# Kernel tuning notes

Hardware: AMD Instinct MI355X
Metric: run time of the kernel (lower is better)

Reference implementation:

```python
import jax, jax.numpy as jnp
import numpy as np

B, T, F, H = 256, 128, 128, 512

def setup_inputs() -> dict:
    key = jax.random.key(0)
    ks = jax.random.split(key, 20)
    def xavier(k, shape):
        fan_in, fan_out = shape[1], shape[0]
        lim = np.sqrt(6.0 / (fan_in + fan_out)).astype(np.float32)
        return jax.random.uniform(k, shape, jnp.float32, -lim, lim)
    inp = {
        "x": jax.random.normal(ks[0], (B, T, F), jnp.float32),
        "m": (jax.random.uniform(ks[1], (B, T, F)) < 0.8).astype(jnp.float32),
        "d": jax.random.uniform(ks[2], (B, T, F), jnp.float32),
        "target_x": jax.random.normal(ks[3], (B, T, F), jnp.float32),
        "target_mask": (jax.random.uniform(ks[4], (B, T, F)) < 0.2).astype(jnp.float32),
        # TemporalDecay h: W [H,F], b [H]
        "td_h_W": xavier(ks[5], (H, F)), "td_h_b": jnp.zeros((H,), jnp.float32),
        # TemporalDecay x (diag): W [F,F], b [F]
        "td_x_W": xavier(ks[6], (F, F)), "td_x_b": jnp.zeros((F,), jnp.float32),
        # hist_reg Linear(H->F)
        "hist_W": xavier(ks[7], (F, H)), "hist_b": jnp.zeros((F,), jnp.float32),
        "feat_W": xavier(ks[8], (F, F)), "feat_b": jnp.zeros((F,), jnp.float32),
        # weight_combine Linear(2F->F)
        "wc_W": xavier(ks[9], (F, 2 * F)), "wc_b": jnp.zeros((F,), jnp.float32),
        # LSTMCell(2F -> H), PyTorch gate order i,f,g,o
        "W_ih": xavier(ks[10], (4 * H, 2 * F)), "W_hh": xavier(ks[11], (4 * H, H)),
        "b_ih": jnp.zeros((4 * H,), jnp.float32), "b_hh": jnp.zeros((4 * H,), jnp.float32),
    }
    return inp

def _rits_forward(x, m, d, target_x, target_mask,
                  td_h_W, td_h_b, td_x_W, td_x_b,
                  hist_W, hist_b, feat_W, feat_b, wc_W, wc_b,
                  W_ih, W_hh, b_ih, b_hh):
    Bx, Tx, Fx = x.shape
    Hx = td_h_W.shape[0]
    feat_mask = (1.0 - jnp.eye(Fx, dtype=x.dtype))
    feat_Wm_T = (feat_W * feat_mask).T              # [F,F]
    td_x_diag = jnp.diagonal(td_x_W)                # diag mask reduces matmul to elementwise

    def step(carry, inp):
        h, c, loss = carry
        x_t, m_t, d_t, tgt_t, ev_t = inp
        gamma_h = jnp.exp(-jax.nn.relu(d_t @ td_h_W.T + td_h_b))    # [B,H]
        gamma_x = jnp.exp(-jax.nn.relu(d_t * td_x_diag + td_x_b))   # [B,F]
        h = h * gamma_h
        x_hist = h @ hist_W.T + hist_b                              # [B,F]
        x_c = m_t * x_t + (1.0 - m_t) * x_hist
        z_h = x_c @ feat_Wm_T + feat_b
        alpha = jax.nn.sigmoid(jnp.concatenate([gamma_x, m_t], axis=1) @ wc_W.T + wc_b)
        c_h = alpha * z_h + (1.0 - alpha) * x_hist
        c_c = m_t * x_t + (1.0 - m_t) * c_h
        inputs = jnp.concatenate([c_c, m_t], axis=1)                # [B,2F]
        gates = inputs @ W_ih.T + b_ih + h @ W_hh.T + b_hh          # [B,4H]
        i_g, f_g, g_g, o_g = jnp.split(gates, 4, axis=1)
        c = jax.nn.sigmoid(f_g) * c + jax.nn.sigmoid(i_g) * jnp.tanh(g_g)
        h = jax.nn.sigmoid(o_g) * jnp.tanh(c)
        denom = ev_t.sum() + 1e-8
        loss = loss + (((x_hist - tgt_t) ** 2 * ev_t).sum()
                       + ((z_h - tgt_t) ** 2 * ev_t).sum()
                       + ((c_h - tgt_t) ** 2 * ev_t).sum()) / denom
        return (h, c, loss), c_c

    h0 = jnp.zeros((Bx, Hx), x.dtype)
    c0 = jnp.zeros((Bx, Hx), x.dtype)
    tm = lambda a: jnp.swapaxes(a, 0, 1)  # time-major [T,B,F]
    (_, _, loss), imps = jax.lax.scan(
        step, (h0, c0, jnp.float32(0.0)),
        (tm(x), tm(m), tm(d), tm(target_x), tm(target_mask)))
    imputations = jnp.swapaxes(imps, 0, 1)  # [B,T,F]
    return imputations, loss / max(Tx, 1)

def reference(x, m, d, target_x, target_mask,
              td_h_W, td_h_b, td_x_W, td_x_b,
              hist_W, hist_b, feat_W, feat_b, wc_W, wc_b,
              W_ih, W_hh, b_ih, b_hh):
    return _rits_forward(x, m, d, target_x, target_mask,
                         td_h_W, td_h_b, td_x_W, td_x_b,
                         hist_W, hist_b, feat_W, feat_b, wc_W, wc_b,
                         W_ih, W_hh, b_ih, b_hh)
```

## Files before the change

### kernel.cpp

```cpp
#include <hip/hip_runtime.h>

#define DEVINL __device__ __forceinline__

namespace {
constexpr int B = 256, T = 128, F = 128, H = 512;
constexpr int NBLK = 256;
constexpr int NTHR = 1024;

constexpr size_t OFF_NUM    = 0;
constexpr size_t OFF_DEN    = 128;
constexpr size_t OFF_WQCC   = 256;
constexpr size_t OFF_WQH    = OFF_WQCC + 64 * 2048;
constexpr size_t OFF_FSCC   = OFF_WQH + 128 * 2048;
constexpr size_t OFF_FSCHG  = OFF_FSCC + 2048;
constexpr size_t OFF_HISTQ  = OFF_FSCHG + 2048;
constexpr size_t OFF_FSCH   = OFF_HISTQ + 128 * 128;
constexpr size_t OFF_TD2    = OFF_FSCH + 128;
constexpr size_t OFF_FEAT2  = OFF_TD2 + 64 * 512;
constexpr size_t OFF_WC2    = OFF_FEAT2 + 64 * 128;
constexpr size_t OFF_BSUM   = OFF_WC2 + 128 * 128;
constexpr size_t OFF_FDIAG  = OFF_BSUM + 2048;
constexpr size_t WS_WORDS   = OFF_FDIAG + 128;

constexpr float ACT_S  = 15.875f;
constexpr float DEQ_CC = 1.f / (127.f * 15.875f);
constexpr float DEQ_H  = 1.f / (127.f * 127.f);
}

typedef _Float16 h2_t __attribute__((ext_vector_type(2)));

DEVINL h2_t as_h2(unsigned u) { union { unsigned u; h2_t h; } c; c.u = u; return c.h; }
DEVINL unsigned pack2(float a, float b) {
  union { h2_t h; unsigned u; } c;
  c.h = h2_t{(_Float16)a, (_Float16)b};
  return c.u;
}

#if defined(__has_builtin)
#if __has_builtin(__builtin_amdgcn_fdot2)
#define HAVE_FDOT2 1
#endif
#if __has_builtin(__builtin_amdgcn_sdot4)
#define HAVE_SDOT4 1
#endif
#endif
#ifdef HAVE_FDOT2
DEVINL float fdot2(h2_t a, h2_t b, float c) { return __builtin_amdgcn_fdot2(a, b, c, false); }
#else
DEVINL float fdot2(h2_t a, h2_t b, float c) {
  return fmaf((float)a.x, (float)b.x, fmaf((float)a.y, (float)b.y, c));
}
#endif
#ifdef HAVE_SDOT4
DEVINL int sdot4(int a, int b, int c) { return __builtin_amdgcn_sdot4(a, b, c, false); }
#else
DEVINL int sdot4(int a, int b, int c) {
  return c + ((a << 24) >> 24) * ((b << 24) >> 24)
           + ((a << 16) >> 24) * ((b << 16) >> 24)
           + ((a << 8) >> 24) * ((b << 8) >> 24)
           + (a >> 24) * (b >> 24);
}
#endif

DEVINL float fast_sig(float x)  { return 1.f / (1.f + __expf(-x)); }
DEVINL float fast_tanh(float x) { return 1.f - 2.f / (1.f + __expf(2.f * x)); }

DEVINL float wave_sum(float v) {
#pragma unroll
  for (int s = 32; s; s >>= 1) v += __shfl_down(v, s, 64);
  return v;
}
DEVINL float wave_max(float v) {
#pragma unroll
  for (int s = 32; s; s >>= 1) v = fmaxf(v, __shfl_down(v, s, 64));
  return v;
}

__global__ void prep_f16(const float* __restrict__ td_h_W, const float* __restrict__ feat_W,
                         const float* __restrict__ wc_W, const float* __restrict__ b_ih,
                         const float* __restrict__ b_hh,
                         unsigned* __restrict__ wsu, float* __restrict__ wsf) {
  int idx = blockIdx.x * blockDim.x + threadIdx.x;
  if (idx < 32768) {
    const int k2 = idx >> 9, j = idx & 511;
    wsu[OFF_TD2 + idx] = pack2(td_h_W[j * 128 + 2 * k2], td_h_W[j * 128 + 2 * k2 + 1]);
  } else if (idx < 40960) {
    const int i = idx - 32768, k2 = i >> 7, f = i & 127;
    wsu[OFF_FEAT2 + i] = pack2(feat_W[f * 128 + 2 * k2], feat_W[f * 128 + 2 * k2 + 1]);
  } else if (idx < 57344) {
    const int i = idx - 40960, k2 = i >> 7, f = i & 127;
    wsu[OFF_WC2 + i] = pack2(wc_W[f * 256 + 2 * k2], wc_W[f * 256 + 2 * k2 + 1]);
  } else if (idx < 59392) {
    const int i = idx - 57344, unit = i >> 2, g = i & 3;
    wsf[OFF_BSUM + i] = b_ih[g * 512 + unit] + b_hh[g * 512 + unit];
  } else if (idx < 59520) {
    const int f = idx - 59392;
    wsf[OFF_FDIAG + f] = (float)(_Float16)feat_W[f * 129];
  }
}

__global__ void prep_quant_wih(const float* __restrict__ Wih,
                               unsigned* __restrict__ wq, float* __restrict__ fscc) {
  const int col = blockIdx.x;
  const int unit = col >> 2, g = col & 3;
  const float* src = Wih + (size_t)(g * 512 + unit) * 256;
  const int t = threadIdx.x;
  const float4 v = ((const float4*)src)[t];
  float mx = fmaxf(fmaxf(fabsf(v.x), fabsf(v.y)), fmaxf(fabsf(v.z), fabsf(v.w)));
  mx = wave_max(mx);
  mx = __shfl(mx, 0, 64);
  const float s = (mx > 0.f) ? 127.f / mx : 0.f;
  const int q0 = __float2int_rn(v.x * s), q1 = __float2int_rn(v.y * s);
  const int q2 = __float2int_rn(v.z * s), q3 = __float2int_rn(v.w * s);
  wq[t * 2048 + col] =
      (q0 & 0xFF) | ((q1 & 0xFF) << 8) | ((q2 & 0xFF) << 16) | ((q3 & 0xFF) << 24);
  if (t == 0) fscc[col] = mx * DEQ_CC;
}

__global__ void prep_quant_whh(const float* __restrict__ Whh,
                               unsigned* __restrict__ wq, float* __restrict__ fschg) {
  const int col = blockIdx.x;
  const int unit = col >> 2, g = col & 3;
  const float* src = Whh + (size_t)(g * 512 + unit) * 512;
  const int t = threadIdx.x;
  const float4 v = ((const float4*)src)[t];
  float mx = fmaxf(fmaxf(fabsf(v.x), fabsf(v.y)), fmaxf(fabsf(v.z), fabsf(v.w)));
  mx = wave_max(mx);
  __shared__ float wm[2];
  if ((t & 63) == 0) wm[t >> 6] = mx;
  __syncthreads();
  const float maxv = fmaxf(wm[0], wm[1]);
  const float s = (maxv > 0.f) ? 127.f / maxv : 0.f;
  const int q0 = __float2int_rn(v.x * s), q1 = __float2int_rn(v.y * s);
  const int q2 = __float2int_rn(v.z * s), q3 = __float2int_rn(v.w * s);
  wq[t * 2048 + col] =
      (q0 & 0xFF) | ((q1 & 0xFF) << 8) | ((q2 & 0xFF) << 16) | ((q3 & 0xFF) << 24);
  if (t == 0) fschg[col] = maxv * DEQ_H;
}

__global__ void prep_quant_hist(const float* __restrict__ histW,
                                unsigned* __restrict__ histq, float* __restrict__ fsch) {
  const int f = blockIdx.x;
  const float* src = histW + (size_t)f * 512;
  const int t = threadIdx.x;
  const float4 v = ((const float4*)src)[t];
  float mx = fmaxf(fmaxf(fabsf(v.x), fabsf(v.y)), fmaxf(fabsf(v.z), fabsf(v.w)));
  mx = wave_max(mx);
  __shared__ float wm[2];
  if ((t & 63) == 0) wm[t >> 6] = mx;
  __syncthreads();
  const float maxv = fmaxf(wm[0], wm[1]);
  const float s = (maxv > 0.f) ? 127.f / maxv : 0.f;
  const int q0 = __float2int_rn(v.x * s), q1 = __float2int_rn(v.y * s);
  const int q2 = __float2int_rn(v.z * s), q3 = __float2int_rn(v.w * s);
  histq[t * 128 + f] =
      (q0 & 0xFF) | ((q1 & 0xFF) << 8) | ((q2 & 0xFF) << 16) | ((q3 & 0xFF) << 24);
  if (t == 0) fsch[f] = maxv * DEQ_H;
}

__global__ void __launch_bounds__(1024) rits_batch(
    const float* __restrict__ x, const float* __restrict__ m, const float* __restrict__ d,
    const float* __restrict__ tx, const float* __restrict__ tmask,
    const float* __restrict__ td_h_b, const float* __restrict__ td_x_W,
    const float* __restrict__ td_x_b, const float* __restrict__ hist_b,
    const float* __restrict__ feat_b, const float* __restrict__ wc_b,
    const unsigned* __restrict__ wsu, const float* __restrict__ wsf,
    float* __restrict__ num, float* __restrict__ den, float* __restrict__ out)
{
  const int tid = threadIdx.x;
  const int row = blockIdx.x;
  const int unit = tid & 511;
  const int kh = tid >> 9;

  __shared__ unsigned actq[64];
  __shared__ int hq[128];
  __shared__ unsigned d2[64];
  __shared__ unsigned xc2[64];
  __shared__ unsigned gxm2[128];
  __shared__ float xrow[128], mrow[128], drow[128], txrow[128], evrow[128];
  __shared__ int   partI[1024];
  __shared__ float partZ[1024], partA[1024];
  __shared__ int4  partHc[512], partHh[512];
  __shared__ float redA[2], redB[2];

  const float4 bs    = *(const float4*)(wsf + OFF_BSUM + 4 * unit);
  const float4 fscc4 = *(const float4*)(wsf + OFF_FSCC + 4 * unit);
  const float4 fsch4 = *(const float4*)(wsf + OFF_FSCHG + 4 * unit);
  const float tdb = td_h_b[unit];
  const int fc = tid & 127;
  const float hb = hist_b[fc], fb = feat_b[fc], wb = wc_b[fc];
  const float fd = wsf[OFF_FDIAG + fc];
  const float dxw = td_x_W[fc * 129], dxb = td_x_b[fc];
  const float fsch_f = wsf[OFF_FSCH + fc];

  float h0 = 0.f, c0 = 0.f;

  for (int t = 0; t < T; ++t) {
    const int base = (row * T + t) * F;
    float xh_r = 0.f, xc_r = 0.f;

    if (tid < 640) {
      const int a = tid >> 7, f = tid & 127;
      const float v = (a == 0 ? x[base + f] : a == 1 ? m[base + f] : a == 2 ? d[base + f]
                       : a == 3 ? tx[base + f] : tmask[base + f]);
      if      (a == 0) xrow[f]  = v;
      else if (a == 1) mrow[f]  = v;
      else if (a == 2) drow[f]  = v;
      else if (a == 3) txrow[f] = v;
      else             evrow[f] = v;
    } else if (tid < 704) {
      const int k2 = tid - 640;
      d2[k2] = pack2(d[base + 2 * k2], d[base + 2 * k2 + 1]);
    } else if (tid < 768) {
      const int q = tid - 704;
      gxm2[64 + q] = pack2(m[base + 2 * q], m[base + 2 * q + 1]);
    } else if (tid < 800) {
      const int w = tid - 768;
      const int b4 = base + 4 * w;
      const int q0 = __float2int_rn(m[b4] * ACT_S);
      const int q1 = __float2int_rn(m[b4 + 1] * ACT_S);
      const int q2 = __float2int_rn(m[b4 + 2] * ACT_S);
      const int q3 = __float2int_rn(m[b4 + 3] * ACT_S);
      actq[32 + w] =
          (q0 & 0xFF) | ((q1 & 0xFF) << 8) | ((q2 & 0xFF) << 16) | ((q3 & 0xFF) << 24);
    }
    __syncthreads();

    if (tid < 512) {
      float g0 = tdb;
#pragma unroll 8
      for (int k2 = 0; k2 < 64; ++k2)
        g0 = fdot2(as_h2(wsu[OFF_TD2 + (k2 << 9) + tid]), as_h2(d2[k2]), g0);
      h0 *= __expf(-fmaxf(g0, 0.f));
      int q = __float2int_rn(h0 * 127.f);
      const int a1 = __shfl_down(q, 1, 64), a2 = __shfl_down(q, 2, 64), a3 = __shfl_down(q, 3, 64);
      if ((tid & 3) == 0)
        hq[tid >> 2] =
            (q & 0xFF) | ((a1 & 0xFF) << 8) | ((a2 & 0xFF) << 16) | ((a3 & 0xFF) << 24);
    }
    __syncthreads();

    {
      const int kq = tid >> 7;
      int isum = 0;
#pragma unroll 8
      for (int k = 0; k < 16; ++k) {
        const int k4 = kq * 16 + k;
        isum = sdot4((int)wsu[OFF_HISTQ + (k4 << 7) + fc], hq[k4], isum);
      }
      partI[tid] = isum;
    }
    __syncthreads();

    if (tid < 128) {
      int isum = 0;
#pragma unroll
      for (int i = 0; i < 8; ++i) isum += partI[tid + 128 * i];
      xh_r = fmaf((float)isum, fsch_f, hb);
      const float gx = __expf(-fmaxf(fmaf(drow[tid], dxw, dxb), 0.f));
      const float mv = mrow[tid];
      xc_r = mv * xrow[tid] + (1.f - mv) * xh_r;
      const float xcs = __shfl_down(xc_r, 1, 64);
      const float gxs = __shfl_down(gx, 1, 64);
      if (!(tid & 1)) {
        xc2[tid >> 1]  = pack2(xc_r, xcs);
        gxm2[tid >> 1] = pack2(gx, gxs);
      }
    }
    __syncthreads();

    {
      const int kq = tid >> 7;
      float zs = 0.f;
#pragma unroll 8
      for (int k = 0; k < 8; ++k) {
        const int k2 = kq * 8 + k;
        zs = fdot2(as_h2(wsu[OFF_FEAT2 + (k2 << 7) + fc]), as_h2(xc2[k2]), zs);
      }
      partZ[tid] = zs;
      float as = 0.f;
#pragma unroll 8
      for (int k = 0; k < 16; ++k) {
        const int k2 = kq * 16 + k;
        as = fdot2(as_h2(wsu[OFF_WC2 + (k2 << 7) + fc]), as_h2(gxm2[k2]), as);
      }
      partA[tid] = as;
    }
    __syncthreads();

    if (tid < 128) {
      float z = fb, aa = wb;
#pragma unroll
      for (int i = 0; i < 8; ++i) { z += partZ[tid + 128 * i]; aa += partA[tid + 128 * i]; }
      z -= xc_r * fd;
      const float al = fast_sig(aa);
      const float ch = al * z + (1.f - al) * xh_r;
      const float mv = mrow[tid];
      const float cc = mv * xrow[tid] + (1.f - mv) * ch;
      out[base + tid] = cc;
      const float ev = evrow[tid], tg = txrow[tid];
      const float e1 = xh_r - tg, e2 = z - tg, e3 = ch - tg;
      const float s1 = wave_sum(ev * (e1 * e1 + e2 * e2 + e3 * e3));
      const float s2 = wave_sum(ev);
      if ((tid & 63) == 0) { redA[tid >> 6] = s1; redB[tid >> 6] = s2; }
      int qc = __float2int_rn(fminf(fmaxf(cc, -8.f), 8.f) * ACT_S);
      const int c1s = __shfl_down(qc, 1, 64), c2s = __shfl_down(qc, 2, 64), c3s = __shfl_down(qc, 3, 64);
      if (!(tid & 3))
        actq[tid >> 2] =
            (qc & 0xFF) | ((c1s & 0xFF) << 8) | ((c2s & 0xFF) << 16) | ((c3s & 0xFF) << 24);
    }
    __syncthreads();

    {
      if (tid == 1023) {
        atomicAdd(&num[t], redA[0] + redA[1]);
        atomicAdd(&den[t], redB[0] + redB[1]);
      }
      int ci = 0, cf = 0, cg = 0, co = 0;
      const unsigned* wq = wsu + OFF_WQCC + 4 * unit;
#pragma unroll 8
      for (int k = 0; k < 32; ++k) {
        const int k4 = kh * 32 + k;
        const uint4 w = *(const uint4*)(wq + (k4 << 11));
        const int a0 = (int)actq[k4];
        ci = sdot4((int)w.x, a0, ci); cf = sdot4((int)w.y, a0, cf);
        cg = sdot4((int)w.z, a0, cg); co = sdot4((int)w.w, a0, co);
      }
      int hi = 0, hf = 0, hg = 0, ho = 0;
      const unsigned* wh = wsu + OFF_WQH + 4 * unit;
#pragma unroll 8
      for (int k = 0; k < 64; ++k) {
        const int k4 = kh * 64 + k;
        const uint4 w = *(const uint4*)(wh + (k4 << 11));
        const int a0 = hq[k4];
        hi = sdot4((int)w.x, a0, hi); hf = sdot4((int)w.y, a0, hf);
        hg = sdot4((int)w.z, a0, hg); ho = sdot4((int)w.w, a0, ho);
      }
      if (tid >= 512) {
        partHc[unit] = int4{ci, cf, cg, co};
        partHh[unit] = int4{hi, hf, hg, ho};
      }
      __syncthreads();
      if (tid < 512) {
        const int4 pc = partHc[unit], ph = partHh[unit];
        const float ai = bs.x + fscc4.x * (float)(ci + pc.x) + fsch4.x * (float)(hi + ph.x);
        const float af = bs.y + fscc4.y * (float)(cf + pc.y) + fsch4.y * (float)(hf + ph.y);
        const float ag = bs.z + fscc4.z * (float)(cg + pc.z) + fsch4.z * (float)(hg + ph.z);
        const float ao = bs.w + fscc4.w * (float)(co + pc.w) + fsch4.w * (float)(ho + ph.w);
        const float ig = fast_sig(ai), fg = fast_sig(af);
        const float gg = fast_tanh(ag), og = fast_sig(ao);
        c0 = fg * c0 + ig * gg;
        h0 = og * fast_tanh(c0);
      }
    }
    __syncthreads();
  }
}

__global__ void finalize(const float* __restrict__ num, const float* __restrict__ den,
                         float* __restrict__ out) {
  __shared__ float red[2];
  const int t = threadIdx.x;
  float v = num[t] / (den[t] + 1e-8f);
  v = wave_sum(v);
  if ((t & 63) == 0) red[t >> 6] = v;
  __syncthreads();
  if (t == 0) out[(size_t)B * T * F] = (red[0] + red[1]) / (float)T;
}

extern "C" void kernel_launch(void* const* d_in, const int* in_sizes, int n_in,
                              void* d_out, int out_size, void* d_ws, size_t ws_size,
                              hipStream_t stream) {
  const float* x      = (const float*)d_in[0];
  const float* m      = (const float*)d_in[1];
  const float* d      = (const float*)d_in[2];
  const float* tx     = (const float*)d_in[3];
  const float* tmask  = (const float*)d_in[4];
  const float* td_h_W = (const float*)d_in[5];
  const float* td_h_b = (const float*)d_in[6];
  const float* td_x_W = (const float*)d_in[7];
  const float* td_x_b = (const float*)d_in[8];
  const float* hist_W = (const float*)d_in[9];
  const float* hist_b = (const float*)d_in[10];
  const float* feat_W = (const float*)d_in[11];
  const float* feat_b = (const float*)d_in[12];
  const float* wc_W   = (const float*)d_in[13];
  const float* wc_b   = (const float*)d_in[14];
  const float* W_ih   = (const float*)d_in[15];
  const float* W_hh   = (const float*)d_in[16];
  const float* b_ih   = (const float*)d_in[17];
  const float* b_hh   = (const float*)d_in[18];

  float*    wsf = (float*)d_ws;
  unsigned* wsu = (unsigned*)d_ws;
  float*    out = (float*)d_out;

  if (ws_size < WS_WORDS * 4) return;

  hipMemsetAsync(d_ws, 0, 256 * sizeof(float), stream);
  prep_f16<<<dim3((59520 + 255) / 256), dim3(256), 0, stream>>>(
      td_h_W, feat_W, wc_W, b_ih, b_hh, wsu, wsf);
  prep_quant_wih<<<dim3(2048), dim3(64), 0, stream>>>(
      W_ih, wsu + OFF_WQCC, wsf + OFF_FSCC);
  prep_quant_whh<<<dim3(2048), dim3(128), 0, stream>>>(
      W_hh, wsu + OFF_WQH, wsf + OFF_FSCHG);
  prep_quant_hist<<<dim3(128), dim3(128), 0, stream>>>(
      hist_W, wsu + OFF_HISTQ, wsf + OFF_FSCH);
  rits_batch<<<dim3(NBLK), dim3(NTHR), 0, stream>>>(
      x, m, d, tx, tmask, td_h_b, td_x_W, td_x_b, hist_b, feat_b, wc_b,
      wsu, wsf, wsf + OFF_NUM, wsf + OFF_DEN, out);
  finalize<<<dim3(1), dim3(128), 0, stream>>>(wsf + OFF_NUM, wsf + OFF_DEN, out);
}
```

Measured before the change: 2.436 ms.

## Split batch rows across cooperating block groups with MFMA int8 gates and global barriers

The main kernel now has groups of 16 blocks cooperate on 16 batch rows. Each block owns a slice of hidden units and features, keeps its LSTM weight fragments in registers, and computes gate matmuls with int8 MFMA instructions in place of per-thread sdot4 loops. Quantized h and imputed-c activations are exchanged through global memory, with atomic-counter barriers between groups at each timestep. The quantization prep kernels are fused and the weights re-laid out for MFMA fragments. The change aims to cut per-block weight streaming and raise matrix throughput. In exchange it adds several grid-level spin barriers per step and depends on all 256 blocks being co-resident.

Result: slower. 5.335 ms (+119.0%).

```diff
diff --git a/kernel.cpp b/kernel.cpp
--- a/kernel.cpp
+++ b/kernel.cpp
@@ -4,23 +4,25 @@
 
 namespace {
 constexpr int B = 256, T = 128, F = 128, H = 512;
-constexpr int NBLK = 256;
-constexpr int NTHR = 1024;
-
-constexpr size_t OFF_NUM    = 0;
-constexpr size_t OFF_DEN    = 128;
-constexpr size_t OFF_WQCC   = 256;
-constexpr size_t OFF_WQH    = OFF_WQCC + 64 * 2048;
-constexpr size_t OFF_FSCC   = OFF_WQH + 128 * 2048;
-constexpr size_t OFF_FSCHG  = OFF_FSCC + 2048;
-constexpr size_t OFF_HISTQ  = OFF_FSCHG + 2048;
-constexpr size_t OFF_FSCH   = OFF_HISTQ + 128 * 128;
-constexpr size_t OFF_TD2    = OFF_FSCH + 128;
-constexpr size_t OFF_FEAT2  = OFF_TD2 + 64 * 512;
-constexpr size_t OFF_WC2    = OFF_FEAT2 + 64 * 128;
-constexpr size_t OFF_BSUM   = OFF_WC2 + 128 * 128;
-constexpr size_t OFF_FDIAG  = OFF_BSUM + 2048;
-constexpr size_t WS_WORDS   = OFF_FDIAG + 128;
+constexpr int NBLK = 256, NTHR = 1024;
+
+constexpr size_t OFF_NUM   = 0;
+constexpr size_t OFF_DEN   = 128;
+constexpr size_t OFF_CTR   = 256;
+constexpr size_t OFF_WQF   = 320;
+constexpr size_t OFF_FSCC  = OFF_WQF + 393216;
+constexpr size_t OFF_FSCHG = OFF_FSCC + 2048;
+constexpr size_t OFF_HISTQ = OFF_FSCHG + 2048;
+constexpr size_t OFF_FSCH  = OFF_HISTQ + 16384;
+constexpr size_t OFF_TD2   = OFF_FSCH + 128;
+constexpr size_t OFF_FEAT2 = OFF_TD2 + 32768;
+constexpr size_t OFF_WC2   = OFF_FEAT2 + 8192;
+constexpr size_t OFF_BSUM  = OFF_WC2 + 16384;
+constexpr size_t OFF_FDIAG = OFF_BSUM + 2048;
+constexpr size_t OFF_HQB   = OFF_FDIAG + 128;
+constexpr size_t OFF_XCB   = OFF_HQB + 65536;
+constexpr size_t OFF_CCB   = OFF_XCB + 32768;
+constexpr size_t WS_WORDS  = OFF_CCB + 16384;
 
 constexpr float ACT_S  = 15.875f;
 constexpr float DEQ_CC = 1.f / (127.f * 15.875f);
@@ -28,6 +30,7 @@
 }
 
 typedef _Float16 h2_t __attribute__((ext_vector_type(2)));
+typedef int v4i __attribute__((ext_vector_type(4)));
 
 DEVINL h2_t as_h2(unsigned u) { union { unsigned u; h2_t h; } c; c.u = u; return c.h; }
 DEVINL unsigned pack2(float a, float b) {
@@ -76,19 +79,44 @@
   return v;
 }
 
+DEVINL unsigned agload(const unsigned* p) {
+  return __hip_atomic_load(p, __ATOMIC_RELAXED, __HIP_MEMORY_SCOPE_AGENT);
+}
+DEVINL unsigned long long agload64(const unsigned long long* p) {
+  return __hip_atomic_load(p, __ATOMIC_RELAXED, __HIP_MEMORY_SCOPE_AGENT);
+}
+DEVINL void agstore(unsigned* p, unsigned v) {
+  __hip_atomic_store(p, v, __ATOMIC_RELAXED, __HIP_MEMORY_SCOPE_AGENT);
+}
+
+DEVINL void group_barrier(unsigned* ctr, unsigned target) {
+  __syncthreads();
+  if (threadIdx.x == 0) {
+    __threadfence();
+    __hip_atomic_fetch_add(ctr, 1u, __ATOMIC_RELEASE, __HIP_MEMORY_SCOPE_AGENT);
+    unsigned v = __hip_atomic_load(ctr, __ATOMIC_ACQUIRE, __HIP_MEMORY_SCOPE_AGENT);
+    int guard = 0;
+    while (v < target && ++guard < (1 << 24)) {
+      __builtin_amdgcn_s_sleep(1);
+      v = __hip_atomic_load(ctr, __ATOMIC_ACQUIRE, __HIP_MEMORY_SCOPE_AGENT);
+    }
+  }
+  __syncthreads();
+}
+
 __global__ void prep_f16(const float* __restrict__ td_h_W, const float* __restrict__ feat_W,
                          const float* __restrict__ wc_W, const float* __restrict__ b_ih,
                          const float* __restrict__ b_hh,
                          unsigned* __restrict__ wsu, float* __restrict__ wsf) {
-  int idx = blockIdx.x * blockDim.x + threadIdx.x;
+  const int idx = blockIdx.x * blockDim.x + threadIdx.x;
   if (idx < 32768) {
-    const int k2 = idx >> 9, j = idx & 511;
-    wsu[OFF_TD2 + idx] = pack2(td_h_W[j * 128 + 2 * k2], td_h_W[j * 128 + 2 * k2 + 1]);
+    const int u = idx >> 6, k2 = idx & 63;
+    wsu[OFF_TD2 + idx] = pack2(td_h_W[u * 128 + 2 * k2], td_h_W[u * 128 + 2 * k2 + 1]);
   } else if (idx < 40960) {
-    const int i = idx - 32768, k2 = i >> 7, f = i & 127;
+    const int i = idx - 32768, f = i >> 6, k2 = i & 63;
     wsu[OFF_FEAT2 + i] = pack2(feat_W[f * 128 + 2 * k2], feat_W[f * 128 + 2 * k2 + 1]);
   } else if (idx < 57344) {
-    const int i = idx - 40960, k2 = i >> 7, f = i & 127;
+    const int i = idx - 40960, f = i >> 7, k2 = i & 127;
     wsu[OFF_WC2 + i] = pack2(wc_W[f * 256 + 2 * k2], wc_W[f * 256 + 2 * k2 + 1]);
   } else if (idx < 59392) {
     const int i = idx - 57344, unit = i >> 2, g = i & 3;
@@ -99,47 +127,48 @@
   }
 }
 
-__global__ void prep_quant_wih(const float* __restrict__ Wih,
-                               unsigned* __restrict__ wq, float* __restrict__ fscc) {
-  const int col = blockIdx.x;
-  const int unit = col >> 2, g = col & 3;
-  const float* src = Wih + (size_t)(g * 512 + unit) * 256;
-  const int t = threadIdx.x;
-  const float4 v = ((const float4*)src)[t];
-  float mx = fmaxf(fmaxf(fabsf(v.x), fabsf(v.y)), fmaxf(fabsf(v.z), fabsf(v.w)));
-  mx = wave_max(mx);
-  mx = __shfl(mx, 0, 64);
-  const float s = (mx > 0.f) ? 127.f / mx : 0.f;
+DEVINL unsigned q4pack(float4 v, float s) {
   const int q0 = __float2int_rn(v.x * s), q1 = __float2int_rn(v.y * s);
   const int q2 = __float2int_rn(v.z * s), q3 = __float2int_rn(v.w * s);
-  wq[t * 2048 + col] =
-      (q0 & 0xFF) | ((q1 & 0xFF) << 8) | ((q2 & 0xFF) << 16) | ((q3 & 0xFF) << 24);
-  if (t == 0) fscc[col] = mx * DEQ_CC;
-}
-
-__global__ void prep_quant_whh(const float* __restrict__ Whh,
-                               unsigned* __restrict__ wq, float* __restrict__ fschg) {
+  return (q0 & 0xFF) | ((q1 & 0xFF) << 8) | ((q2 & 0xFF) << 16) | ((q3 & 0xFF) << 24);
+}
+
+__global__ void prep_gates(const float* __restrict__ Wih, const float* __restrict__ Whh,
+                           unsigned* __restrict__ wsu, float* __restrict__ wsf) {
   const int col = blockIdx.x;
-  const int unit = col >> 2, g = col & 3;
-  const float* src = Whh + (size_t)(g * 512 + unit) * 512;
-  const int t = threadIdx.x;
-  const float4 v = ((const float4*)src)[t];
-  float mx = fmaxf(fmaxf(fabsf(v.x), fabsf(v.y)), fmaxf(fabsf(v.z), fabsf(v.w)));
-  mx = wave_max(mx);
-  __shared__ float wm[2];
-  if ((t & 63) == 0) wm[t >> 6] = mx;
-  __syncthreads();
-  const float maxv = fmaxf(wm[0], wm[1]);
-  const float s = (maxv > 0.f) ? 127.f / maxv : 0.f;
-  const int q0 = __float2int_rn(v.x * s), q1 = __float2int_rn(v.y * s);
-  const int q2 = __float2int_rn(v.z * s), q3 = __float2int_rn(v.w * s);
-  wq[t * 2048 + col] =
-      (q0 & 0xFF) | ((q1 & 0xFF) << 8) | ((q2 & 0xFF) << 16) | ((q3 & 0xFF) << 24);
-  if (t == 0) fschg[col] = maxv * DEQ_H;
-}
-
-__global__ void prep_quant_hist(const float* __restrict__ histW,
-                                unsigned* __restrict__ histq, float* __restrict__ fsch) {
+  const int unit = col >> 2, g = col & 3, t = threadIdx.x;
+  const float* si = Wih + (size_t)(g * 512 + unit) * 256;
+  const float* sh = Whh + (size_t)(g * 512 + unit) * 512;
+  const float4 vi = ((const float4*)si)[t];
+  const float4 va = ((const float4*)sh)[t];
+  const float4 vb = ((const float4*)sh)[t + 64];
+  float mi = fmaxf(fmaxf(fabsf(vi.x), fabsf(vi.y)), fmaxf(fabsf(vi.z), fabsf(vi.w)));
+  float mh = fmaxf(fmaxf(fmaxf(fabsf(va.x), fabsf(va.y)), fmaxf(fabsf(va.z), fabsf(va.w))),
+                   fmaxf(fmaxf(fabsf(vb.x), fabsf(vb.y)), fmaxf(fabsf(vb.z), fabsf(vb.w))));
+  mi = wave_max(mi); mh = wave_max(mh);
+  mi = __shfl(mi, 0, 64); mh = __shfl(mh, 0, 64);
+  const float ssi = (mi > 0.f) ? 127.f / mi : 0.f;
+  const float ssh = (mh > 0.f) ? 127.f / mh : 0.f;
+  if (t == 0) { wsf[OFF_FSCC + col] = mi * DEQ_CC; wsf[OFF_FSCHG + col] = mh * DEQ_H; }
+
+  const int mid = col >> 7, nl = (col >> 4) & 7, c15 = col & 15;
+  const int q = (t >> 2) & 3, r = t & 3;
+  {
+    const int kt = t >> 4, kh = kt >> 1, loc = (kt & 1) * 4 + r;
+    const size_t a = ((size_t)((((mid * 8 + nl) * 2 + kh) * 64) + q * 16 + c15)) * 24 + loc;
+    wsu[OFF_WQF + a] = q4pack(vi, ssi);
+  }
+#pragma unroll
+  for (int p = 0; p < 2; ++p) {
+    const int k4 = t + 64 * p;
+    const int kt = k4 >> 4, kh = kt >> 2, loc = 8 + (kt & 3) * 4 + r;
+    const size_t a = ((size_t)((((mid * 8 + nl) * 2 + kh) * 64) + q * 16 + c15)) * 24 + loc;
+    wsu[OFF_WQF + a] = q4pack(p ? vb : va, ssh);
+  }
+}
+
+__global__ void prep_hist(const float* __restrict__ histW,
+                          unsigned* __restrict__ wsu, float* __restrict__ wsf) {
   const int f = blockIdx.x;
   const float* src = histW + (size_t)f * 512;
   const int t = threadIdx.x;
@@ -151,207 +180,276 @@
   __syncthreads();
   const float maxv = fmaxf(wm[0], wm[1]);
   const float s = (maxv > 0.f) ? 127.f / maxv : 0.f;
-  const int q0 = __float2int_rn(v.x * s), q1 = __float2int_rn(v.y * s);
-  const int q2 = __float2int_rn(v.z * s), q3 = __float2int_rn(v.w * s);
-  histq[t * 128 + f] =
-      (q0 & 0xFF) | ((q1 & 0xFF) << 8) | ((q2 & 0xFF) << 16) | ((q3 & 0xFF) << 24);
-  if (t == 0) fsch[f] = maxv * DEQ_H;
-}
-
-__global__ void __launch_bounds__(1024) rits_batch(
+  wsu[OFF_HISTQ + (size_t)f * 128 + t] = q4pack(v, s);
+  if (t == 0) wsf[OFF_FSCH + f] = maxv * DEQ_H;
+}
+
+__global__ void __launch_bounds__(NTHR) rits_group(
     const float* __restrict__ x, const float* __restrict__ m, const float* __restrict__ d,
     const float* __restrict__ tx, const float* __restrict__ tmask,
     const float* __restrict__ td_h_b, const float* __restrict__ td_x_W,
     const float* __restrict__ td_x_b, const float* __restrict__ hist_b,
     const float* __restrict__ feat_b, const float* __restrict__ wc_b,
-    const unsigned* __restrict__ wsu, const float* __restrict__ wsf,
+    unsigned* __restrict__ ws, const float* __restrict__ wsf,
     float* __restrict__ num, float* __restrict__ den, float* __restrict__ out)
 {
   const int tid = threadIdx.x;
-  const int row = blockIdx.x;
-  const int unit = tid & 511;
-  const int kh = tid >> 9;
-
-  __shared__ unsigned actq[64];
-  __shared__ int hq[128];
-  __shared__ unsigned d2[64];
-  __shared__ unsigned xc2[64];
-  __shared__ unsigned gxm2[128];
-  __shared__ float xrow[128], mrow[128], drow[128], txrow[128], evrow[128];
-  __shared__ int   partI[1024];
-  __shared__ float partZ[1024], partA[1024];
-  __shared__ int4  partHc[512], partHh[512];
-  __shared__ float redA[2], redB[2];
-
-  const float4 bs    = *(const float4*)(wsf + OFF_BSUM + 4 * unit);
-  const float4 fscc4 = *(const float4*)(wsf + OFF_FSCC + 4 * unit);
-  const float4 fsch4 = *(const float4*)(wsf + OFF_FSCHG + 4 * unit);
-  const float tdb = td_h_b[unit];
-  const int fc = tid & 127;
-  const float hb = hist_b[fc], fb = feat_b[fc], wb = wc_b[fc];
-  const float fd = wsf[OFF_FDIAG + fc];
-  const float dxw = td_x_W[fc * 129], dxb = td_x_b[fc];
-  const float fsch_f = wsf[OFF_FSCH + fc];
-
-  float h0 = 0.f, c0 = 0.f;
+  const int grp = blockIdx.x & 15, mid = blockIdx.x >> 4;
+  const int r0g = grp << 4, u0 = mid << 5, f0 = mid << 3, c0 = mid << 7;
+  const int lane = tid & 63, wv = tid >> 6;
+  const int nl = wv >> 1, kh = wv & 1;
+  const int m15 = lane & 15, lg = lane >> 4, swA = (m15 & 3) << 2;
+
+  __shared__ __align__(16) unsigned tdl_s[32 * 68];
+  __shared__ __align__(16) unsigned histl_s[8 * 132];
+  __shared__ __align__(16) unsigned featl_s[8 * 68];
+  __shared__ __align__(16) unsigned wcl_s[8 * 132];
+  __shared__ __align__(16) unsigned hq_s[16 * 132];
+  __shared__ __align__(16) unsigned actq_s[16 * 68];
+  __shared__ float h_s[16 * 33], c_s[16 * 33];
+  __shared__ float dxw_s[128], dxb_s[128];
+  __shared__ __align__(16) unsigned arena32[4800];
+
+  unsigned* d2_a   = arena32;
+  unsigned* xc2_a  = arena32 + 1088;
+  unsigned* gxm2_a = arena32 + 2176;
+  float* xsl  = (float*)(arena32 + 4288);
+  float* txsl = (float*)(arena32 + 4416);
+  float* evsl = (float*)(arena32 + 4544);
+  float* msl  = (float*)(arena32 + 4672);
+  float* gb   = (float*)arena32;
+
+  const unsigned* wqf = ws + OFF_WQF +
+      (size_t)((((mid << 3) + nl) * 2 + kh) * 64 + lane) * 24;
+  const v4i bcc0 = *(const v4i*)(wqf + 0),  bcc1 = *(const v4i*)(wqf + 4);
+  const v4i bh0  = *(const v4i*)(wqf + 8),  bh1  = *(const v4i*)(wqf + 12);
+  const v4i bh2  = *(const v4i*)(wqf + 16), bh3  = *(const v4i*)(wqf + 20);
+
+  const int colg = c0 + (nl << 4) + m15;
+  const float fscc_r = wsf[OFF_FSCC + colg];
+  const float fsch_r = wsf[OFF_FSCHG + colg];
+  const float bs_r   = wsf[OFF_BSUM + colg];
+
+  float tdb = 0.f;
+  if (tid < 512) tdb = td_h_b[u0 + (tid >> 4)];
+  float hb = 0.f, fb = 0.f, wb = 0.f, fd = 0.f, fsf = 0.f;
+  if (tid < 128) {
+    const int f = f0 + (tid & 7);
+    hb = hist_b[f]; fb = feat_b[f]; wb = wc_b[f];
+    fd = wsf[OFF_FDIAG + f]; fsf = wsf[OFF_FSCH + f];
+  }
+
+  {
+    if (tid < 512) {
+      const int u = tid >> 4, w4 = (tid & 15) << 2;
+#pragma unroll
+      for (int i = 0; i < 4; ++i)
+        tdl_s[u * 68 + w4 + i] = ws[OFF_TD2 + (size_t)(u0 + u) * 64 + w4 + i];
+      featl_s[(tid >> 6) * 68 + (tid & 63)] =
+          ws[OFF_FEAT2 + (size_t)(f0 + (tid >> 6)) * 64 + (tid & 63)];
+    }
+    histl_s[(tid >> 7) * 132 + (tid & 127)] =
+        ws[OFF_HISTQ + (size_t)(f0 + (tid >> 7)) * 128 + (tid & 127)];
+    wcl_s[(tid >> 7) * 132 + (tid & 127)] =
+        ws[OFF_WC2 + (size_t)(f0 + (tid >> 7)) * 128 + (tid & 127)];
+    if (tid < 128) { dxw_s[tid] = td_x_W[tid * 129]; dxb_s[tid] = td_x_b[tid]; }
+    if (tid < 528) { h_s[tid] = 0.f; c_s[tid] = 0.f; }
+  }
+  __syncthreads();
+
+  unsigned* ctr = ws + OFF_CTR + grp * 3;
 
   for (int t = 0; t < T; ++t) {
-    const int base = (row * T + t) * F;
-    float xh_r = 0.f, xc_r = 0.f;
-
-    if (tid < 640) {
-      const int a = tid >> 7, f = tid & 127;
-      const float v = (a == 0 ? x[base + f] : a == 1 ? m[base + f] : a == 2 ? d[base + f]
-                       : a == 3 ? tx[base + f] : tmask[base + f]);
-      if      (a == 0) xrow[f]  = v;
-      else if (a == 1) mrow[f]  = v;
-      else if (a == 2) drow[f]  = v;
-      else if (a == 3) txrow[f] = v;
-      else             evrow[f] = v;
-    } else if (tid < 704) {
-      const int k2 = tid - 640;
-      d2[k2] = pack2(d[base + 2 * k2], d[base + 2 * k2 + 1]);
-    } else if (tid < 768) {
-      const int q = tid - 704;
-      gxm2[64 + q] = pack2(m[base + 2 * q], m[base + 2 * q + 1]);
-    } else if (tid < 800) {
-      const int w = tid - 768;
-      const int b4 = base + 4 * w;
-      const int q0 = __float2int_rn(m[b4] * ACT_S);
-      const int q1 = __float2int_rn(m[b4 + 1] * ACT_S);
-      const int q2 = __float2int_rn(m[b4 + 2] * ACT_S);
-      const int q3 = __float2int_rn(m[b4 + 3] * ACT_S);
-      actq[32 + w] =
-          (q0 & 0xFF) | ((q1 & 0xFF) << 8) | ((q2 & 0xFF) << 16) | ((q3 & 0xFF) << 24);
+    const int par = t & 1;
+    unsigned* hqb = ws + OFF_HQB + (size_t)((par * 16 + grp) * 16) * 128;
+    unsigned* xcb = ws + OFF_XCB + (size_t)((par * 16 + grp) * 16) * 64;
+    unsigned* ccb = ws + OFF_CCB + (size_t)((par * 16 + grp) * 16) * 32;
+    const unsigned tgt = 16u * (unsigned)(t + 1);
+
+    float xh = 0.f, xc = 0.f, mvv = 0.f, xvv = 0.f;
+
+    {
+      const int r = tid >> 6, j = tid & 63;
+      const size_t base = ((size_t)(r0g + r) * T + t) * F;
+      const float dv0 = d[base + 2 * j], dv1 = d[base + 2 * j + 1];
+      d2_a[r * 68 + j] = pack2(dv0, dv1);
+      const float gx0 = __expf(-fmaxf(fmaf(dv0, dxw_s[2 * j], dxb_s[2 * j]), 0.f));
+      const float gx1 = __expf(-fmaxf(fmaf(dv1, dxw_s[2 * j + 1], dxb_s[2 * j + 1]), 0.f));
+      gxm2_a[r * 132 + j] = pack2(gx0, gx1);
+      const float mv0 = m[base + 2 * j], mv1 = m[base + 2 * j + 1];
+      gxm2_a[r * 132 + 64 + j] = pack2(mv0, mv1);
+      if (j < 32) {
+        const int q0 = __float2int_rn(m[base + 4 * j] * ACT_S);
+        const int q1 = __float2int_rn(m[base + 4 * j + 1] * ACT_S);
+        const int q2 = __float2int_rn(m[base + 4 * j + 2] * ACT_S);
+        const int q3 = __float2int_rn(m[base + 4 * j + 3] * ACT_S);
+        actq_s[r * 68 + ((32 + j) ^ ((r & 3) << 2))] =
+            (q0 & 0xFF) | ((q1 & 0xFF) << 8) | ((q2 & 0xFF) << 16) | ((q3 & 0xFF) << 24);
+        const int k = j & 7, sel = j >> 3;
+        const float v = (sel == 0) ? x[base + f0 + k] : (sel == 1) ? tx[base + f0 + k]
+                      : (sel == 2) ? tmask[base + f0 + k] : m[base + f0 + k];
+        if (sel == 0) xsl[r * 8 + k] = v;
+        else if (sel == 1) txsl[r * 8 + k] = v;
+        else if (sel == 2) evsl[r * 8 + k] = v;
+        else msl[r * 8 + k] = v;
+      }
     }
     __syncthreads();
 
     if (tid < 512) {
+      const int u = tid >> 4, r = tid & 15;
       float g0 = tdb;
+      const uint4* tw = (const uint4*)(tdl_s + u * 68);
+      const uint4* dw = (const uint4*)(d2_a + r * 68);
+#pragma unroll
+      for (int q = 0; q < 16; ++q) {
+        const uint4 w = tw[q], dd = dw[q];
+        g0 = fdot2(as_h2(w.x), as_h2(dd.x), g0);
+        g0 = fdot2(as_h2(w.y), as_h2(dd.y), g0);
+        g0 = fdot2(as_h2(w.z), as_h2(dd.z), g0);
+        g0 = fdot2(as_h2(w.w), as_h2(dd.w), g0);
+      }
+      const float hv = h_s[r * 33 + u] * __expf(-fmaxf(g0, 0.f));
+      h_s[r * 33 + u] = hv;
+      int q = __float2int_rn(hv * 127.f);
+      const int a1 = __shfl_down(q, 16, 64), a2 = __shfl_down(q, 32, 64),
+                a3 = __shfl_down(q, 48, 64);
+      if (!(u & 3))
+        agstore(hqb + r * 128 + (u0 >> 2) + (u >> 2),
+                (q & 0xFF) | ((a1 & 0xFF) << 8) | ((a2 & 0xFF) << 16) | ((a3 & 0xFF) << 24));
+    }
+    group_barrier(ctr + 0, tgt);
+
+    {
+      const int r = tid >> 6, w0 = (tid & 63) << 1;
+      const unsigned long long v =
+          agload64((const unsigned long long*)(hqb + r * 128 + w0));
+      const int swr = (r & 3) << 2;
+      hq_s[r * 132 + (w0 ^ swr)] = (unsigned)v;
+      hq_s[r * 132 + ((w0 | 1) ^ swr)] = (unsigned)(v >> 32);
+    }
+    __syncthreads();
+
+    if (tid < 128) {
+      const int r = tid >> 3, fl = tid & 7;
+      int isum = 0;
+      const uint4* hw = (const uint4*)(histl_s + fl * 132);
+      const int swr = (r & 3) << 2;
 #pragma unroll 8
-      for (int k2 = 0; k2 < 64; ++k2)
-        g0 = fdot2(as_h2(wsu[OFF_TD2 + (k2 << 9) + tid]), as_h2(d2[k2]), g0);
-      h0 *= __expf(-fmaxf(g0, 0.f));
-      int q = __float2int_rn(h0 * 127.f);
-      const int a1 = __shfl_down(q, 1, 64), a2 = __shfl_down(q, 2, 64), a3 = __shfl_down(q, 3, 64);
-      if ((tid & 3) == 0)
-        hq[tid >> 2] =
-            (q & 0xFF) | ((a1 & 0xFF) << 8) | ((a2 & 0xFF) << 16) | ((a3 & 0xFF) << 24);
+      for (int qq = 0; qq < 32; ++qq) {
+        const uint4 w = hw[qq];
+        const int4 hv = *(const int4*)(hq_s + r * 132 + (((qq) << 2) ^ swr));
+        isum = sdot4((int)w.x, hv.x, isum);
+        isum = sdot4((int)w.y, hv.y, isum);
+        isum = sdot4((int)w.z, hv.z, isum);
+        isum = sdot4((int)w.w, hv.w, isum);
+      }
+      xh = fmaf((float)isum, fsf, hb);
+      mvv = msl[r * 8 + fl]; xvv = xsl[r * 8 + fl];
+      xc = mvv * xvv + (1.f - mvv) * xh;
+      const float xcs = __shfl_down(xc, 1, 64);
+      if (!(fl & 1)) agstore(xcb + r * 64 + ((f0 + fl) >> 1), pack2(xc, xcs));
+    }
+    group_barrier(ctr + 1, tgt);
+
+    {
+      const int r = tid >> 6, w = tid & 63;
+      xc2_a[r * 68 + w] = agload(xcb + r * 64 + w);
     }
     __syncthreads();
 
+    if (tid < 128) {
+      const int r = tid >> 3, fl = tid & 7;
+      float z = fb, aa = wb;
+      {
+        const uint4* fw = (const uint4*)(featl_s + fl * 68);
+        const uint4* xw = (const uint4*)(xc2_a + r * 68);
+#pragma unroll 8
+        for (int qq = 0; qq < 16; ++qq) {
+          const uint4 w = fw[qq], x4 = xw[qq];
+          z = fdot2(as_h2(w.x), as_h2(x4.x), z);
+          z = fdot2(as_h2(w.y), as_h2(x4.y), z);
+          z = fdot2(as_h2(w.z), as_h2(x4.z), z);
+          z = fdot2(as_h2(w.w), as_h2(x4.w), z);
+        }
+        const uint4* ww = (const uint4*)(wcl_s + fl * 132);
+        const uint4* gw = (const uint4*)(gxm2_a + r * 132);
+#pragma unroll 8
+        for (int qq = 0; qq < 32; ++qq) {
+          const uint4 w = ww[qq], g4 = gw[qq];
+          aa = fdot2(as_h2(w.x), as_h2(g4.x), aa);
+          aa = fdot2(as_h2(w.y), as_h2(g4.y), aa);
+          aa = fdot2(as_h2(w.z), as_h2(g4.z), aa);
+          aa = fdot2(as_h2(w.w), as_h2(g4.w), aa);
+        }
+      }
+      z -= xc * fd;
+      const float al = fast_sig(aa);
+      const float ch = al * z + (1.f - al) * xh;
+      const float cc = mvv * xvv + (1.f - mvv) * ch;
+      out[((size_t)(r0g + r) * T + t) * F + f0 + fl] = cc;
+      const float tg = txsl[r * 8 + fl], evv = evsl[r * 8 + fl];
+      const float e1 = xh - tg, e2 = z - tg, e3 = ch - tg;
+      const float s1 = wave_sum(evv * (e1 * e1 + e2 * e2 + e3 * e3));
+      const float s2 = wave_sum(evv);
+      if (!(tid & 63)) { atomicAdd(&num[t], s1); atomicAdd(&den[t], s2); }
+      int qc = __float2int_rn(fminf(fmaxf(cc, -8.f), 8.f) * ACT_S);
+      const int c1 = __shfl_down(qc, 1, 64), c2 = __shfl_down(qc, 2, 64),
+                c3 = __shfl_down(qc, 3, 64);
+      if (!(fl & 3))
+        agstore(ccb + r * 32 + ((f0 + fl) >> 2),
+                (qc & 0xFF) | ((c1 & 0xFF) << 8) | ((c2 & 0xFF) << 16) | ((c3 & 0xFF) << 24));
+    }
+
+    v4i accH = {0, 0, 0, 0};
     {
-      const int kq = tid >> 7;
-      int isum = 0;
-#pragma unroll 8
-      for (int k = 0; k < 16; ++k) {
-        const int k4 = kq * 16 + k;
-        isum = sdot4((int)wsu[OFF_HISTQ + (k4 << 7) + fc], hq[k4], isum);
+      const unsigned* hrow = hq_s + m15 * 132;
+      const v4i a0 = *(const v4i*)(hrow + ((((kh * 4 + 0) << 4) + (lg << 2)) ^ swA));
+      accH = __builtin_amdgcn_mfma_i32_16x16x64_i8(a0, bh0, accH, 0, 0, 0);
+      const v4i a1 = *(const v4i*)(hrow + ((((kh * 4 + 1) << 4) + (lg << 2)) ^ swA));
+      accH = __builtin_amdgcn_mfma_i32_16x16x64_i8(a1, bh1, accH, 0, 0, 0);
+      const v4i a2 = *(const v4i*)(hrow + ((((kh * 4 + 2) << 4) + (lg << 2)) ^ swA));
+      accH = __builtin_amdgcn_mfma_i32_16x16x64_i8(a2, bh2, accH, 0, 0, 0);
+      const v4i a3 = *(const v4i*)(hrow + ((((kh * 4 + 3) << 4) + (lg << 2)) ^ swA));
+      accH = __builtin_amdgcn_mfma_i32_16x16x64_i8(a3, bh3, accH, 0, 0, 0);
+    }
+    group_barrier(ctr + 2, tgt);
+
+    if (tid < 512) {
+      const int r = tid >> 5, w = tid & 31;
+      actq_s[r * 68 + (w ^ ((r & 3) << 2))] = agload(ccb + r * 32 + w);
+    }
+    __syncthreads();
+
+    {
+      v4i accC = {0, 0, 0, 0};
+      const unsigned* arow = actq_s + m15 * 68;
+      const v4i a0 = *(const v4i*)(arow + ((((kh * 2 + 0) << 4) + (lg << 2)) ^ swA));
+      accC = __builtin_amdgcn_mfma_i32_16x16x64_i8(a0, bcc0, accC, 0, 0, 0);
+      const v4i a1 = *(const v4i*)(arow + ((((kh * 2 + 1) << 4) + (lg << 2)) ^ swA));
+      accC = __builtin_amdgcn_mfma_i32_16x16x64_i8(a1, bcc1, accC, 0, 0, 0);
+      float* gbp = gb + (size_t)((kh << 7) + (nl << 4) + m15) * 18 + (lg << 2);
+      const float badd = kh ? 0.f : bs_r;
+      gbp[0] = fmaf(fscc_r, (float)accC[0], fmaf(fsch_r, (float)accH[0], badd));
+      gbp[1] = fmaf(fscc_r, (float)accC[1], fmaf(fsch_r, (float)accH[1], badd));
+      gbp[2] = fmaf(fscc_r, (float)accC[2], fmaf(fsch_r, (float)accH[2], badd));
+      gbp[3] = fmaf(fscc_r, (float)accC[3], fmaf(fsch_r, (float)accH[3], badd));
+    }
+    __syncthreads();
+
+    if (tid < 512) {
+      const int ul = tid >> 4, r = tid & 15;
+      float a4[4];
+#pragma unroll
+      for (int gg = 0; gg < 4; ++gg) {
+        const int cl = ul * 4 + gg;
+        a4[gg] = gb[(size_t)cl * 18 + r] + gb[(size_t)(128 + cl) * 18 + r];
       }
-      partI[tid] = isum;
-    }
-    __syncthreads();
-
-    if (tid < 128) {
-      int isum = 0;
-#pragma unroll
-      for (int i = 0; i < 8; ++i) isum += partI[tid + 128 * i];
-      xh_r = fmaf((float)isum, fsch_f, hb);
-      const float gx = __expf(-fmaxf(fmaf(drow[tid], dxw, dxb), 0.f));
-      const float mv = mrow[tid];
-      xc_r = mv * xrow[tid] + (1.f - mv) * xh_r;
-      const float xcs = __shfl_down(xc_r, 1, 64);
-      const float gxs = __shfl_down(gx, 1, 64);
-      if (!(tid & 1)) {
-        xc2[tid >> 1]  = pack2(xc_r, xcs);
-        gxm2[tid >> 1] = pack2(gx, gxs);
-      }
-    }
-    __syncthreads();
-
-    {
-      const int kq = tid >> 7;
-      float zs = 0.f;
-#pragma unroll 8
-      for (int k = 0; k < 8; ++k) {
-        const int k2 = kq * 8 + k;
-        zs = fdot2(as_h2(wsu[OFF_FEAT2 + (k2 << 7) + fc]), as_h2(xc2[k2]), zs);
-      }
-      partZ[tid] = zs;
-      float as = 0.f;
-#pragma unroll 8
-      for (int k = 0; k < 16; ++k) {
-        const int k2 = kq * 16 + k;
-        as = fdot2(as_h2(wsu[OFF_WC2 + (k2 << 7) + fc]), as_h2(gxm2[k2]), as);
-      }
-      partA[tid] = as;
-    }
-    __syncthreads();
-
-    if (tid < 128) {
-      float z = fb, aa = wb;
-#pragma unroll
-      for (int i = 0; i < 8; ++i) { z += partZ[tid + 128 * i]; aa += partA[tid + 128 * i]; }
-      z -= xc_r * fd;
-      const float al = fast_sig(aa);
-      const float ch = al * z + (1.f - al) * xh_r;
-      const float mv = mrow[tid];
-      const float cc = mv * xrow[tid] + (1.f - mv) * ch;
-      out[base + tid] = cc;
-      const float ev = evrow[tid], tg = txrow[tid];
-      const float e1 = xh_r - tg, e2 = z - tg, e3 = ch - tg;
-      const float s1 = wave_sum(ev * (e1 * e1 + e2 * e2 + e3 * e3));
-      const float s2 = wave_sum(ev);
-      if ((tid & 63) == 0) { redA[tid >> 6] = s1; redB[tid >> 6] = s2; }
-      int qc = __float2int_rn(fminf(fmaxf(cc, -8.f), 8.f) * ACT_S);
-      const int c1s = __shfl_down(qc, 1, 64), c2s = __shfl_down(qc, 2, 64), c3s = __shfl_down(qc, 3, 64);
-      if (!(tid & 3))
-        actq[tid >> 2] =
-            (qc & 0xFF) | ((c1s & 0xFF) << 8) | ((c2s & 0xFF) << 16) | ((c3s & 0xFF) << 24);
-    }
-    __syncthreads();
-
-    {
-      if (tid == 1023) {
-        atomicAdd(&num[t], redA[0] + redA[1]);
-        atomicAdd(&den[t], redB[0] + redB[1]);
-      }
-      int ci = 0, cf = 0, cg = 0, co = 0;
-      const unsigned* wq = wsu + OFF_WQCC + 4 * unit;
-#pragma unroll 8
-      for (int k = 0; k < 32; ++k) {
-        const int k4 = kh * 32 + k;
-        const uint4 w = *(const uint4*)(wq + (k4 << 11));
-        const int a0 = (int)actq[k4];
-        ci = sdot4((int)w.x, a0, ci); cf = sdot4((int)w.y, a0, cf);
-        cg = sdot4((int)w.z, a0, cg); co = sdot4((int)w.w, a0, co);
-      }
-      int hi = 0, hf = 0, hg = 0, ho = 0;
-      const unsigned* wh = wsu + OFF_WQH + 4 * unit;
-#pragma unroll 8
-      for (int k = 0; k < 64; ++k) {
-        const int k4 = kh * 64 + k;
-        const uint4 w = *(const uint4*)(wh + (k4 << 11));
-        const int a0 = hq[k4];
-        hi = sdot4((int)w.x, a0, hi); hf = sdot4((int)w.y, a0, hf);
-        hg = sdot4((int)w.z, a0, hg); ho = sdot4((int)w.w, a0, ho);
-      }
-      if (tid >= 512) {
-        partHc[unit] = int4{ci, cf, cg, co};
-        partHh[unit] = int4{hi, hf, hg, ho};
-      }
-      __syncthreads();
-      if (tid < 512) {
-        const int4 pc = partHc[unit], ph = partHh[unit];
-        const float ai = bs.x + fscc4.x * (float)(ci + pc.x) + fsch4.x * (float)(hi + ph.x);
-        const float af = bs.y + fscc4.y * (float)(cf + pc.y) + fsch4.y * (float)(hf + ph.y);
-        const float ag = bs.z + fscc4.z * (float)(cg + pc.z) + fsch4.z * (float)(hg + ph.z);
-        const float ao = bs.w + fscc4.w * (float)(co + pc.w) + fsch4.w * (float)(ho + ph.w);
-        const float ig = fast_sig(ai), fg = fast_sig(af);
-        const float gg = fast_tanh(ag), og = fast_sig(ao);
-        c0 = fg * c0 + ig * gg;
-        h0 = og * fast_tanh(c0);
-      }
+      const float ig = fast_sig(a4[0]), fg = fast_sig(a4[1]);
+      const float g2 = fast_tanh(a4[2]), og = fast_sig(a4[3]);
+      const float cv = fg * c_s[r * 33 + ul] + ig * g2;
+      c_s[r * 33 + ul] = cv;
+      h_s[r * 33 + ul] = og * fast_tanh(cv);
     }
     __syncthreads();
   }
@@ -391,22 +489,17 @@
   const float* b_ih   = (const float*)d_in[17];
   const float* b_hh   = (const float*)d_in[18];
 
+  unsigned* wsu = (unsigned*)d_ws;
   float*    wsf = (float*)d_ws;
-  unsigned* wsu = (unsigned*)d_ws;
   float*    out = (float*)d_out;
 
   if (ws_size < WS_WORDS * 4) return;
 
-  hipMemsetAsync(d_ws, 0, 256 * sizeof(float), stream);
-  prep_f16<<<dim3((59520 + 255) / 256), dim3(256), 0, stream>>>(
-      td_h_W, feat_W, wc_W, b_ih, b_hh, wsu, wsf);
-  prep_quant_wih<<<dim3(2048), dim3(64), 0, stream>>>(
-      W_ih, wsu + OFF_WQCC, wsf + OFF_FSCC);
-  prep_quant_whh<<<dim3(2048), dim3(128), 0, stream>>>(
-      W_hh, wsu + OFF_WQH, wsf + OFF_FSCHG);
-  prep_quant_hist<<<dim3(128), dim3(128), 0, stream>>>(
-      hist_W, wsu + OFF_HISTQ, wsf + OFF_FSCH);
-  rits_batch<<<dim3(NBLK), dim3(NTHR), 0, stream>>>(
+  hipMemsetAsync(d_ws, 0, (OFF_CTR + 64) * 4, stream);
+  prep_f16<<<dim3(233), dim3(256), 0, stream>>>(td_h_W, feat_W, wc_W, b_ih, b_hh, wsu, wsf);
+  prep_gates<<<dim3(2048), dim3(64), 0, stream>>>(W_ih, W_hh, wsu, wsf);
+  prep_hist<<<dim3(128), dim3(128), 0, stream>>>(hist_W, wsu, wsf);
+  rits_group<<<dim3(NBLK), dim3(NTHR), 0, stream>>>(
       x, m, d, tx, tmask, td_h_b, td_x_W, td_x_b, hist_b, feat_b, wc_b,
       wsu, wsf, wsf + OFF_NUM, wsf + OFF_DEN, out);
   finalize<<<dim3(1), dim3(128), 0, stream>>>(wsf + OFF_NUM, wsf + OFF_DEN, out);
```
